# Optimization experiments

Hardware: AMD Instinct MI355X
Metric: run time of the kernel (lower is better)

## Reference

```python
import jax, jax.numpy as jnp
import numpy as np

B, H, S, D = 2, 8, 2048, 64
WINDOW = 3            # local_attention_window (default in torch forward)
FRAC = 0.3            # percentage_frac hardcoded in create_window_tensor call
MASK_FILL = -1.0e9


def window_kernel(window, frac):
    # create_window_tensor: [ (1-f)^n ... (1-f)^1, 1, (1-f)^1 ... (1-f)^n ]
    n = (window - 1) // 2
    side = np.array([(1.0 - frac) ** i for i in range(n, 0, -1)], dtype=np.float32)
    vals = np.concatenate([side, np.array([1.0], np.float32), side[::-1]])
    return jnp.asarray(vals)


def setup_inputs() -> dict:
    key = jax.random.key(0)
    kq, kk, kv = jax.random.split(key, 3)
    queries = jax.random.normal(kq, (B, H, S, D), jnp.float32)
    keys = jax.random.normal(kk, (B, H, S, D), jnp.float32)
    values = jax.random.normal(kv, (B, H, S, D), jnp.float32)
    # causal mask: True positions are filled with -1e9 (masked_fill semantics)
    mask = jnp.triu(jnp.ones((S, S), dtype=bool), 1)[None, None]  # [1,1,S,S]
    # linear_bias: nn.Parameter(torch.zeros(Sk)) created inside forward
    beta = jnp.zeros((S,), jnp.float32)
    return {"queries": queries, "keys": keys, "values": values,
            "beta": beta, "mask": mask}


def reference(queries, keys, values, beta, mask):
    d = keys.shape[-1]
    # scores = Q K^T / sqrt(d)
    scores = jnp.einsum("bhqd,bhkd->bhqk", queries, keys) / jnp.sqrt(
        jnp.asarray(d, queries.dtype))
    scores = jnp.where(mask, jnp.asarray(MASK_FILL, scores.dtype), scores)
    # include_local_attention=True, local_attention_dim_vertical=False:
    # the torch code transposes, conv2d with a [1,W] kernel along the last
    # axis, transposes back -> 1D cross-correlation along the QUERY axis.
    # Kernel is symmetric so correlation == convolution. Zero padding.
    kern = window_kernel(WINDOW, FRAC)
    p = (WINDOW - 1) // 2
    xp = jnp.pad(scores, ((0, 0), (0, 0), (p, p), (0, 0)))
    Sq = scores.shape[2]
    scores = sum(kern[i] * jax.lax.dynamic_slice_in_dim(xp, i, Sq, axis=2)
                 for i in range(WINDOW))
    # linear_bias=True: add zero-initialized per-key-position bias
    scores = scores + beta  # broadcasts over last dim [Sk]
    weights = jax.nn.softmax(scores, axis=-1)
    return jnp.einsum("bhqk,bhkd->bhqd", weights, values)
```

## Files before the change

kernel.cpp:

```cpp
#include <hip/hip_runtime.h>


typedef short bf16x8 __attribute__((ext_vector_type(8)));
typedef float f32x4  __attribute__((ext_vector_type(4)));

constexpr int S_ = 2048;
constexpr int D_ = 64;
constexpr float LOG2E = 1.44269504088896341f;
constexpr float KSC = 0.125f * LOG2E;

__device__ __forceinline__ unsigned pk2(float lo, float hi) {
    union { float f; unsigned u; } a, b;
    a.f = lo; b.f = hi;
    return __builtin_amdgcn_perm(b.u + 0x8000u, a.u + 0x8000u, 0x07060302u);
}

__global__ __launch_bounds__(256)
void cvt_frag(const float* __restrict__ K, const float* __restrict__ V,
              unsigned short* __restrict__ F)
{
    const int tid  = blockIdx.x * 256 + threadIdx.x;
    const int lane = tid & 63;
    const int frag = (tid >> 6) & 15;
    const int tt   = (tid >> 10) & 31;
    const int hd   = tid >> 15;
    const int n_l = lane & 15, qd = lane >> 4;
    unsigned w[4];
    if (frag < 8) {
        const int kh = frag >> 2, mb = (frag >> 1) & 1, hh = frag & 1;
        const int key = tt * 64 + kh * 32 + ((n_l >> 2) << 3) + (n_l & 3) + mb * 4;
        const int d0  = hh * 32 + qd * 8;
        const float* src = K + (size_t)(hd * S_ + key) * D_ + d0;
        float4 a = *(const float4*)src;
        float4 b = *(const float4*)(src + 4);
        w[0] = pk2(a.x, a.y); w[1] = pk2(a.z, a.w);
        w[2] = pk2(b.x, b.y); w[3] = pk2(b.z, b.w);
    } else {
        const int kh = (frag >> 2) & 1, mb = frag & 3;
        const int key0 = tt * 64 + kh * 32 + qd * 8;
        const int d = mb * 16 + n_l;
        const float* src = V + (size_t)(hd * S_ + key0) * D_ + d;
        float e[8];
        #pragma unroll
        for (int j = 0; j < 8; ++j) e[j] = src[j * D_];
        w[0] = pk2(e[0], e[1]); w[1] = pk2(e[2], e[3]);
        w[2] = pk2(e[4], e[5]); w[3] = pk2(e[6], e[7]);
    }
    *(uint4*)(F + (size_t)tid * 8) = make_uint4(w[0], w[1], w[2], w[3]);
}

__global__ __launch_bounds__(512, 2)
void attn7(const float* __restrict__ Q, const float* __restrict__ beta,
           const unsigned short* __restrict__ F, float* __restrict__ out)
{
    __shared__ float opub[4][16][68];
    __shared__ float lred[4][16];

    const int bid = blockIdx.x;
    const int hd = bid & 15;
    const int pr = bid >> 4;

    const float* Qh = Q + (size_t)hd * S_ * D_;
    const unsigned short* Fh = F + (size_t)hd * 32 * 16 * 512;

    const int t = threadIdx.x, lane = t & 63;
    const int wv = t >> 6, kh = wv & 1, sg = wv >> 1;
    const int n_l = lane & 15, qd = lane >> 4;

    const int lo = lane * 8;
    int kfo[2][2], vfo[4];
    #pragma unroll
    for (int mb = 0; mb < 2; ++mb)
        #pragma unroll
        for (int hh = 0; hh < 2; ++hh)
            kfo[mb][hh] = ((kh << 2) | (mb << 1) | hh) * 512 + lo;
    #pragma unroll
    for (int mb = 0; mb < 4; ++mb)
        vfo[mb] = (8 + (kh << 2) + mb) * 512 + lo;

    const int kvo = (kh << 5) + (qd << 3);
    const float* bp = beta + kvo;

    for (int p = 0; p < 2; ++p) {
        const int j = p ? (31 - pr) : pr;
        const int q0 = j << 6;
        const int nt = j + 1;
        const int qbase = q0 + (sg << 4);
        const int qr = qbase + n_l;

        auto ld = [&](int tile, bf16x8 (&ka)[2][2], bf16x8 (&vb)[4], float (&bt)[8]) {
            const unsigned short* fp = Fh + (size_t)tile * 8192;
            ka[0][0] = *(const bf16x8*)(fp + kfo[0][0]);
            ka[0][1] = *(const bf16x8*)(fp + kfo[0][1]);
            ka[1][0] = *(const bf16x8*)(fp + kfo[1][0]);
            ka[1][1] = *(const bf16x8*)(fp + kfo[1][1]);
            #pragma unroll
            for (int mb = 0; mb < 4; ++mb)
                vb[mb] = *(const bf16x8*)(fp + vfo[mb]);
            const float* bq = bp + (tile << 6);
            float4 b0 = *(const float4*)(bq);
            float4 b1 = *(const float4*)(bq + 4);
            bt[0] = b0.x * LOG2E; bt[1] = b0.y * LOG2E;
            bt[2] = b0.z * LOG2E; bt[3] = b0.w * LOG2E;
            bt[4] = b1.x * LOG2E; bt[5] = b1.y * LOG2E;
            bt[6] = b1.z * LOG2E; bt[7] = b1.w * LOG2E;
        };

        bf16x8 kaA[2][2], vbA[4]; float btA[8];
        bf16x8 kaB[2][2], vbB[4]; float btB[8];
        ld(0, kaA, vbA, btA);
        if (nt > 1) ld(1, kaB, vbB, btB);

        bf16x8 qb[2];
        {
            const float wp = (qr > 0) ? 0.7f : 0.0f;
            const float wn = (qr + 1 < S_) ? 0.7f : 0.0f;
            const float* qc = Qh + (size_t)qr * D_;
            const float* qpp = qc - ((qr > 0) ? D_ : 0);
            const float* qnn = qc + ((qr + 1 < S_) ? D_ : 0);
            #pragma unroll
            for (int hh = 0; hh < 2; ++hh) {
                const int d0 = (hh << 5) + (qd << 3);
                float4 c0 = *(const float4*)(qc + d0),  c1 = *(const float4*)(qc + d0 + 4);
                float4 p0 = *(const float4*)(qpp + d0), p1 = *(const float4*)(qpp + d0 + 4);
                float4 n0 = *(const float4*)(qnn + d0), n1 = *(const float4*)(qnn + d0 + 4);
                float e0 = fmaf(wn, n0.x, fmaf(wp, p0.x, c0.x));
                float e1 = fmaf(wn, n0.y, fmaf(wp, p0.y, c0.y));
                float e2 = fmaf(wn, n0.z, fmaf(wp, p0.z, c0.z));
                float e3 = fmaf(wn, n0.w, fmaf(wp, p0.w, c0.w));
                float e4 = fmaf(wn, n1.x, fmaf(wp, p1.x, c1.x));
                float e5 = fmaf(wn, n1.y, fmaf(wp, p1.y, c1.y));
                float e6 = fmaf(wn, n1.z, fmaf(wp, p1.z, c1.z));
                float e7 = fmaf(wn, n1.w, fmaf(wp, p1.w, c1.w));
                union { unsigned u[4]; bf16x8 v; } qu;
                qu.u[0] = pk2(e0, e1); qu.u[1] = pk2(e2, e3);
                qu.u[2] = pk2(e4, e5); qu.u[3] = pk2(e6, e7);
                qb[hh] = qu.v;
            }
        }

        f32x4 o[4];
        float l = 0.0f;
        #pragma unroll
        for (int mb = 0; mb < 4; ++mb) o[mb] = (f32x4){0, 0, 0, 0};

        auto comp = [&](int tile, bf16x8 (&ka)[2][2], bf16x8 (&vb)[4], float (&bt)[8]) {
            const f32x4 zz = {0, 0, 0, 0};
            f32x4 acc[2];
            #pragma unroll
            for (int mb = 0; mb < 2; ++mb) {
                f32x4 a = __builtin_amdgcn_mfma_f32_16x16x32_bf16(ka[mb][0], qb[0], zz, 0, 0, 0);
                acc[mb] = __builtin_amdgcn_mfma_f32_16x16x32_bf16(ka[mb][1], qb[1], a, 0, 0, 0);
            }
            const bool dm = (tile == nt - 1);
            const int kk = (tile << 6) + kvo;
            float pv[8];
            float la = 0.0f;
            #pragma unroll
            for (int jj = 0; jj < 8; ++jj) {
                const int mb = jj >> 2, r = jj & 3;
                float sv = fmaf(acc[mb][r], KSC, bt[jj]);
                if (dm) {
                    const int key = kk + jj;
                    if (!((key < qr) || (qr == 0 && key == 0))) sv = -1.0e30f;
                }
                pv[jj] = __builtin_amdgcn_exp2f(sv);
                la += pv[jj];
            }
            l += la;
            union { unsigned u[4]; bf16x8 v; } pf;
            pf.u[0] = pk2(pv[0], pv[1]);
            pf.u[1] = pk2(pv[2], pv[3]);
            pf.u[2] = pk2(pv[4], pv[5]);
            pf.u[3] = pk2(pv[6], pv[7]);
            #pragma unroll
            for (int mb = 0; mb < 4; ++mb)
                o[mb] = __builtin_amdgcn_mfma_f32_16x16x32_bf16(vb[mb], pf.v, o[mb], 0, 0, 0);
        };

        int it = 0;
        for (; it + 2 <= nt; it += 2) {
            comp(it, kaA, vbA, btA);
            if (it + 2 < nt) ld(it + 2, kaA, vbA, btA);
            comp(it + 1, kaB, vbB, btB);
            if (it + 3 < nt) ld(it + 3, kaB, vbB, btB);
        }
        if (it < nt) comp(it, kaA, vbA, btA);

        l += __shfl_xor(l, 16);
        l += __shfl_xor(l, 32);
        __syncthreads();
        if (kh == 0) {
            #pragma unroll
            for (int mb = 0; mb < 4; ++mb)
                *(float4*)&opub[sg][n_l][(mb << 4) + (qd << 2)] =
                    make_float4(o[mb][0], o[mb][1], o[mb][2], o[mb][3]);
            if (qd == 0) lred[sg][n_l] = l;
        }
        __syncthreads();
        if (kh == 1) {
            const float inv = 1.0f / (l + lred[sg][n_l]);
            float* op = out + ((size_t)hd * S_ + qr) * D_ + (qd << 2);
            #pragma unroll
            for (int mb = 0; mb < 4; ++mb) {
                float4 pv = *(float4*)&opub[sg][n_l][(mb << 4) + (qd << 2)];
                *(float4*)(op + (mb << 4)) =
                    make_float4((o[mb][0] + pv.x) * inv, (o[mb][1] + pv.y) * inv,
                                (o[mb][2] + pv.z) * inv, (o[mb][3] + pv.w) * inv);
            }
        }
    }
}

extern "C" void kernel_launch(void* const* d_in, const int* in_sizes, int n_in,
                              void* d_out, int out_size, void* d_ws, size_t ws_size,
                              hipStream_t stream) {
    const float* Q    = (const float*)d_in[0];
    const float* K    = (const float*)d_in[1];
    const float* V    = (const float*)d_in[2];
    const float* beta = (const float*)d_in[3];
    float* out = (float*)d_out;

    unsigned short* F = (unsigned short*)d_ws;

    cvt_frag<<<dim3(2048), 256, 0, stream>>>(K, V, F);
    attn7<<<dim3(256), 512, 0, stream>>>(Q, beta, F, out);
}
```

Measured before the change: 118.0 us.

## Transpose V through shared memory in conversion and deepen attention prefetch to three stages

The K/V conversion kernel now processes one 64-key tile per block, reading K and V rows with coalesced float4 loads and transposing V through shared memory. This replaces the previous strided 8-element column reads of V. The attention kernel moves from double-buffered to triple-buffered fragment prefetch, loading the tile two iterations ahead. That gives more latency hiding at the cost of extra registers under the 512-thread, 2-block launch bound.

```diff
diff --git a/kernel.cpp b/kernel.cpp
--- a/kernel.cpp
+++ b/kernel.cpp
@@ -16,41 +16,64 @@
 }
 
 __global__ __launch_bounds__(256)
-void cvt_frag(const float* __restrict__ K, const float* __restrict__ V,
-              unsigned short* __restrict__ F)
+void cvt8(const float* __restrict__ K, const float* __restrict__ V,
+          unsigned short* __restrict__ F)
 {
-    const int tid  = blockIdx.x * 256 + threadIdx.x;
-    const int lane = tid & 63;
-    const int frag = (tid >> 6) & 15;
-    const int tt   = (tid >> 10) & 31;
-    const int hd   = tid >> 15;
-    const int n_l = lane & 15, qd = lane >> 4;
-    unsigned w[4];
-    if (frag < 8) {
-        const int kh = frag >> 2, mb = (frag >> 1) & 1, hh = frag & 1;
-        const int key = tt * 64 + kh * 32 + ((n_l >> 2) << 3) + (n_l & 3) + mb * 4;
-        const int d0  = hh * 32 + qd * 8;
-        const float* src = K + (size_t)(hd * S_ + key) * D_ + d0;
-        float4 a = *(const float4*)src;
-        float4 b = *(const float4*)(src + 4);
-        w[0] = pk2(a.x, a.y); w[1] = pk2(a.z, a.w);
-        w[2] = pk2(b.x, b.y); w[3] = pk2(b.z, b.w);
-    } else {
-        const int kh = (frag >> 2) & 1, mb = frag & 3;
-        const int key0 = tt * 64 + kh * 32 + qd * 8;
-        const int d = mb * 16 + n_l;
-        const float* src = V + (size_t)(hd * S_ + key0) * D_ + d;
-        float e[8];
+    __shared__ float T[64][68];
+
+    const int bid = blockIdx.x;
+    const int hd = bid & 15, tt = bid >> 4;
+    const float* Kt = K + ((size_t)hd * S_ + tt * 64) * D_;
+    const float* Vt = V + ((size_t)hd * S_ + tt * 64) * D_;
+    unsigned short* Ft = F + (size_t)(hd * 32 + tt) * 8192;
+
+    const int t = threadIdx.x;
+    const int key = t >> 2, d0 = (t & 3) << 4;
+
+    {
+        const float* vp = Vt + key * D_ + d0;
         #pragma unroll
-        for (int j = 0; j < 8; ++j) e[j] = src[j * D_];
-        w[0] = pk2(e[0], e[1]); w[1] = pk2(e[2], e[3]);
-        w[2] = pk2(e[4], e[5]); w[3] = pk2(e[6], e[7]);
-    }
-    *(uint4*)(F + (size_t)tid * 8) = make_uint4(w[0], w[1], w[2], w[3]);
+        for (int i = 0; i < 4; ++i) {
+            float4 v4 = *(const float4*)(vp + 4 * i);
+            T[d0 + 4 * i + 0][key] = v4.x;
+            T[d0 + 4 * i + 1][key] = v4.y;
+            T[d0 + 4 * i + 2][key] = v4.z;
+            T[d0 + 4 * i + 3][key] = v4.w;
+        }
+    }
+
+    {
+        const float* kp = Kt + key * D_ + d0;
+        float4 a = *(const float4*)(kp);
+        float4 b = *(const float4*)(kp + 4);
+        float4 c = *(const float4*)(kp + 8);
+        float4 d = *(const float4*)(kp + 12);
+        uint4 w0 = make_uint4(pk2(a.x, a.y), pk2(a.z, a.w), pk2(b.x, b.y), pk2(b.z, b.w));
+        uint4 w1 = make_uint4(pk2(c.x, c.y), pk2(c.z, c.w), pk2(d.x, d.y), pk2(d.z, d.w));
+        const int r5 = key & 31;
+        const int kh = key >> 5, mb = (r5 >> 2) & 1;
+        const int n = ((r5 >> 3) << 2) | (r5 & 3);
+        const int hh = d0 >> 5, qd0 = (d0 >> 3) & 3;
+        const int f0 = (kh << 2) | (mb << 1) | hh;
+        *(uint4*)(Ft + f0 * 512 + ((qd0 << 4) | n) * 8)       = w0;
+        *(uint4*)(Ft + f0 * 512 + (((qd0 + 1) << 4) | n) * 8) = w1;
+    }
+    __syncthreads();
+
+    #pragma unroll
+    for (int s = 0; s < 2; ++s) {
+        const int slot = t + s * 256;
+        const int fr = slot >> 6, lane = slot & 63;
+        const int kh = fr >> 2, mb = fr & 3, n = lane & 15, qd = lane >> 4;
+        const float* row = &T[mb * 16 + n][kh * 32 + qd * 8];
+        uint4 w = make_uint4(pk2(row[0], row[1]), pk2(row[2], row[3]),
+                             pk2(row[4], row[5]), pk2(row[6], row[7]));
+        *(uint4*)(Ft + (8 + fr) * 512 + lane * 8) = w;
+    }
 }
 
 __global__ __launch_bounds__(512, 2)
-void attn7(const float* __restrict__ Q, const float* __restrict__ beta,
+void attn8(const float* __restrict__ Q, const float* __restrict__ beta,
            const unsigned short* __restrict__ F, float* __restrict__ out)
 {
     __shared__ float opub[4][16][68];
@@ -61,7 +84,7 @@
     const int pr = bid >> 4;
 
     const float* Qh = Q + (size_t)hd * S_ * D_;
-    const unsigned short* Fh = F + (size_t)hd * 32 * 16 * 512;
+    const unsigned short* Fh = F + (size_t)hd * 32 * 8192;
 
     const int t = threadIdx.x, lane = t & 63;
     const int wv = t >> 6, kh = wv & 1, sg = wv >> 1;
@@ -108,6 +131,7 @@
 
         bf16x8 kaA[2][2], vbA[4]; float btA[8];
         bf16x8 kaB[2][2], vbB[4]; float btB[8];
+        bf16x8 kaC[2][2], vbC[4]; float btC[8];
         ld(0, kaA, vbA, btA);
         if (nt > 1) ld(1, kaB, vbB, btB);
 
@@ -179,13 +203,16 @@
         };
 
         int it = 0;
-        for (; it + 2 <= nt; it += 2) {
+        for (; it + 3 <= nt; it += 3) {
+            ld(it + 2, kaC, vbC, btC);
             comp(it, kaA, vbA, btA);
-            if (it + 2 < nt) ld(it + 2, kaA, vbA, btA);
+            if (it + 3 < nt) ld(it + 3, kaA, vbA, btA);
             comp(it + 1, kaB, vbB, btB);
-            if (it + 3 < nt) ld(it + 3, kaB, vbB, btB);
-        }
-        if (it < nt) comp(it, kaA, vbA, btA);
+            if (it + 4 < nt) ld(it + 4, kaB, vbB, btB);
+            comp(it + 2, kaC, vbC, btC);
+        }
+        if (it < nt)     comp(it, kaA, vbA, btA);
+        if (it + 1 < nt) comp(it + 1, kaB, vbB, btB);
 
         l += __shfl_xor(l, 16);
         l += __shfl_xor(l, 32);
@@ -223,6 +250,6 @@
 
     unsigned short* F = (unsigned short*)d_ws;
 
-    cvt_frag<<<dim3(2048), 256, 0, stream>>>(K, V, F);
-    attn7<<<dim3(256), 512, 0, stream>>>(Q, beta, F, out);
-}
+    cvt8<<<dim3(512), 256, 0, stream>>>(K, V, F);
+    attn8<<<dim3(256), 512, 0, stream>>>(Q, beta, F, out);
+}
```

Result: no change. 118.2 us (+0.1%).
